# Kernel optimization log

Measured on AMD Instinct MI355X. Metric: run time of the kernel, lower is better.

The kernel has to match this reference:

```python
import jax, jax.numpy as jnp
from jax import lax
import numpy as np

NC = 3              # immutable color channels
HIDDEN = 16         # hidden state channels
STATE = NC + HIDDEN # 19
PV = 5              # perception vectors per channel
PERC = PV * STATE   # 95
MID = 128


def setup_inputs() -> dict:
    key = jax.random.key(0)
    ks = jax.random.split(key, 7)
    x = jax.random.uniform(ks[0], (4, NC, 128, 128), dtype=jnp.float32)
    # grouped 3x3 conv: groups=STATE, 1 in-ch -> PV out-ch per group; OIHW kernel (95,1,3,3)
    Wp = jax.random.normal(ks[1], (PERC, 1, 3, 3), dtype=jnp.float32) * 0.1
    bp = jax.random.normal(ks[2], (PERC,), dtype=jnp.float32) * 0.01
    W1 = jax.random.normal(ks[3], (MID, PERC), dtype=jnp.float32) * 0.05
    b1 = jax.random.normal(ks[4], (MID,), dtype=jnp.float32) * 0.01
    W2 = jax.random.normal(ks[5], (HIDDEN, MID), dtype=jnp.float32) * 0.05
    b2 = jax.random.normal(ks[6], (HIDDEN,), dtype=jnp.float32) * 0.01
    return {"x": x, "Wp": Wp, "bp": bp, "W1": W1, "b1": b1, "W2": W2, "b2": b2, "steps": 16}


def _maxpool3x3(x):
    # 3x3 stride-1 pad-1 max pool over NCHW spatial dims
    return lax.reduce_window(x, -jnp.inf, lax.max,
                             (1, 1, 3, 3), (1, 1, 1, 1),
                             ((0, 0), (0, 0), (1, 1), (1, 1)))


def reference(x, Wp, bp, W1, b1, W2, b2, steps):
    N, _, H, W = x.shape
    state0 = jnp.concatenate([x, jnp.zeros((N, HIDDEN, H, W), x.dtype)], axis=1)

    def step(state, _):
        # depthwise/grouped 3x3 perception conv (groups = STATE)
        p = lax.conv_general_dilated(state, Wp, (1, 1), ((1, 1), (1, 1)),
                                     feature_group_count=STATE,
                                     dimension_numbers=("NCHW", "OIHW", "NCHW"))
        p = p + bp[None, :, None, None]
        # 1x1 conv -> LeakyReLU(0.2) -> 1x1 conv
        h = jnp.einsum("nchw,oc->nohw", p, W1) + b1[None, :, None, None]
        h = jnp.where(h >= 0, h, 0.2 * h)
        upd = jnp.einsum("nchw,oc->nohw", h, W2) + b2[None, :, None, None]
        # stochastic_update with p=1: mask = rand < 1 is always True -> plain add
        s = state.at[:, NC:].add(upd)
        # alive mask: maxpool of channel 4 > 0 gates all mutable channels
        alive = (_maxpool3x3(s[:, 4:5]) > 0).astype(s.dtype)
        s = s.at[:, NC:].multiply(alive)
        # sigmoid slice-assign on channel 4
        s = s.at[:, 4].set(jax.nn.sigmoid(s[:, 4]))
        return s, None

    final, _ = lax.scan(step, state0, None, length=steps)
    return final
```

## Files before the change

### kernel.cpp

```cpp
#include <hip/hip_runtime.h>
#include <math.h>

#define NN    4
#define NC    3
#define HID   16
#define CST   19
#define PV    5
#define PERC  95
#define MIDC  128
#define HH    128
#define WW    128
#define HW    (HH*WW)
#define STEPS 16
#define TPX   256
#define NTHR  1024
#define KP    104
#define HT    136
#define W1F_N 24576
#define W2F_N 4096

typedef short  bf16x8 __attribute__((ext_vector_type(8)));
typedef float  f32x4v __attribute__((ext_vector_type(4)));

__device__ __forceinline__ unsigned short f2bf_rtn(float f) {
    unsigned u = __float_as_uint(f);
    u += 0x7FFFu + ((u >> 16) & 1u);
    return (unsigned short)(u >> 16);
}
__device__ __forceinline__ float bf2f(unsigned short h) {
    return __uint_as_float(((unsigned)h) << 16);
}
__device__ __forceinline__ void bfsplit(float a, short& hi, short& lo) {
    unsigned short hb = f2bf_rtn(a);
    hi = (short)hb;
    lo = (short)f2bf_rtn(a - bf2f(hb));
}
__device__ __forceinline__ unsigned packsplit(float a) {
    unsigned short hb = f2bf_rtn(a);
    unsigned short lb = f2bf_rtn(a - bf2f(hb));
    return ((unsigned)hb << 16) | (unsigned)lb;
}

__global__ __launch_bounds__(1024) void nca_wprep(
        short* __restrict__ wf,
        const float* __restrict__ W1, const float* __restrict__ W2) {
    const int tid = threadIdx.x;
    for (int e = tid; e < W1F_N; e += 1024) {
        int j = e & 7, lane = (e >> 3) & 63, q = e >> 9;
        int ch = q % 12, wrow = q / 12;
        int hl = ch & 1, t = ch >> 1, ks = t % 3, mt = t / 3;
        int lw = lane & 15, g = lane >> 4;
        int m  = wrow * 32 + mt * 16 + lw;
        int kk = ks * 32 + g * 8 + j;
        float av = (kk < PERC) ? W1[m * PERC + kk] : 0.0f;
        short hi, lo; bfsplit(av, hi, lo);
        wf[e] = hl ? lo : hi;
    }
    for (int e = tid; e < W2F_N; e += 1024) {
        int j = e & 7, lane = (e >> 3) & 63, q = e >> 9;
        int hl = q & 1, ks = q >> 1;
        int lw = lane & 15, g = lane >> 4;
        float av = W2[lw * MIDC + ks * 32 + g * 8 + j];
        short hi, lo; bfsplit(av, hi, lo);
        wf[W1F_N + e] = hl ? lo : hi;
    }
}

__global__ __launch_bounds__(NTHR) void nca_fused(
        const float* __restrict__ tmp_in,  long istride,
        float* __restrict__ tmp_out,       long ostride,
        const float* __restrict__ x,
        const short* __restrict__ wscr,
        const float* __restrict__ Wp, const float* __restrict__ bp,
        const float* __restrict__ b1, const float* __restrict__ b2,
        int first) {
    const int tile    = ((blockIdx.x & 7) << 5) + (blockIdx.x >> 3);
    const int n       = tile >> 6;
    const int pixbase = (tile & 63) * TPX;
    const int y0      = pixbase >> 7;
    const int tid     = threadIdx.x;
    const int lane    = tid & 63;
    const int w       = __builtin_amdgcn_readfirstlane(tid >> 6);
    const int wrow    = w >> 2;
    const int wcol    = w & 3;
    const int lw      = lane & 15;
    const int g       = lane >> 4;
    const int g8      = g * 8;

    __shared__ __align__(16) unsigned char raw[139840];
    unsigned* pp    = (unsigned*)raw;
    unsigned* hp    = (unsigned*)raw;
    float*    stile = (float*)(raw + 106496);
    float*    b1tab = (float*)(raw + 139264);
    float*    b2tab = (float*)(raw + 139776);

    if (tid < MIDC) b1tab[tid] = b1[tid];
    else if (tid < MIDC + HID) b2tab[tid - MIDC] = b2[tid - MIDC];

    {
        const int u2   = tid & 511;
        const int half = tid >> 9;
        const int px   = u2 & 127;
        const int yy   = y0 - 1 + (u2 >> 7);
        if (!first && yy >= 0 && yy < HH) {
            const float* tb = tmp_in + (size_t)n * istride;
            const float* c1 = tb + 1 * HW;
            const int idx = (yy << 7) + px;
            const bool ym = (yy > 0), yp = (yy < HH - 1);
            const bool xm = (px > 0), xp = (px < WW - 1);
            float mx = c1[idx];
            if (ym)       mx = fmaxf(mx, c1[idx - WW]);
            if (yp)       mx = fmaxf(mx, c1[idx + WW]);
            if (xm)       mx = fmaxf(mx, c1[idx - 1]);
            if (xp)       mx = fmaxf(mx, c1[idx + 1]);
            if (ym && xm) mx = fmaxf(mx, c1[idx - WW - 1]);
            if (ym && xp) mx = fmaxf(mx, c1[idx - WW + 1]);
            if (yp && xm) mx = fmaxf(mx, c1[idx + WW - 1]);
            if (yp && xp) mx = fmaxf(mx, c1[idx + WW + 1]);
            const float alive = (mx > 0.0f) ? 1.0f : 0.0f;
#pragma unroll
            for (int cc = 0; cc < 8; ++cc) {
                const int c = half * 8 + cc;
                float v = tb[c * HW + idx] * alive;
                if (c == 1) v = 1.0f / (1.0f + expf(-v));
                stile[c * 512 + u2] = v;
            }
        } else {
#pragma unroll
            for (int cc = 0; cc < 8; ++cc)
                stile[(half * 8 + cc) * 512 + u2] = 0.0f;
        }
    }

    bf16x8 ah[2][3], al[2][3];
#pragma unroll
    for (int mt = 0; mt < 2; ++mt)
#pragma unroll
        for (int ks = 0; ks < 3; ++ks) {
            const int base = ((wrow * 12 + ((mt * 3 + ks) << 1)) * 64 + lane) * 8;
            ah[mt][ks] = *(const bf16x8*)&wscr[base];
            al[mt][ks] = *(const bf16x8*)&wscr[base + 512];
        }

    auto conv_emit = [&](int c, int p, float t00, float t01, float t02,
                         float t10, float t11, float t12,
                         float t20, float t21, float t22) {
#pragma unroll
        for (int v = 0; v < PV; ++v) {
            const float* wv = Wp + (c * PV + v) * 9;
            float a = bp[c * PV + v];
            a += wv[0] * t00; a += wv[1] * t01; a += wv[2] * t02;
            a += wv[3] * t10; a += wv[4] * t11; a += wv[5] * t12;
            a += wv[6] * t20; a += wv[7] * t21; a += wv[8] * t22;
            pp[p * KP + c * PV + v] = packsplit(a);
        }
    };

    if (tid < 768) {
        const int c = tid >> 8;
        const int p = tid & 255;
        const int y = y0 + (p >> 7);
        const int xc = p & 127;
        const bool xm = (xc > 0), xp = (xc < WW - 1);
        const int gpix = (y << 7) + xc;
        const float* ch = x + ((size_t)n * NC + c) * HW;
        const bool ym = (y > 0), yp = (y < HH - 1);
        float t00 = (ym && xm) ? ch[gpix - WW - 1] : 0.0f;
        float t01 = ym         ? ch[gpix - WW]     : 0.0f;
        float t02 = (ym && xp) ? ch[gpix - WW + 1] : 0.0f;
        float t10 = xm         ? ch[gpix - 1]      : 0.0f;
        float t11 =              ch[gpix];
        float t12 = xp         ? ch[gpix + 1]      : 0.0f;
        float t20 = (yp && xm) ? ch[gpix + WW - 1] : 0.0f;
        float t21 = yp         ? ch[gpix + WW]     : 0.0f;
        float t22 = (yp && xp) ? ch[gpix + WW + 1] : 0.0f;
        conv_emit(c, p, t00, t01, t02, t10, t11, t12, t20, t21, t22);
    }
    if (tid < 256) pp[tid * KP + 95] = 0;
    __syncthreads();

#pragma unroll
    for (int it = 0; it < 4; ++it) {
        const int u = 768 + it * NTHR + tid;
        const int c = u >> 8;
        const int p = u & 255;
        const int xc = p & 127;
        const bool xm = (xc > 0), xp = (xc < WW - 1);
        const float* sr = stile + (c - NC) * 512;
        const int b = ((p >> 7) + 1) * 128 + xc;
        float t00 = xm ? sr[b - 128 - 1] : 0.0f;
        float t01 =      sr[b - 128];
        float t02 = xp ? sr[b - 128 + 1] : 0.0f;
        float t10 = xm ? sr[b - 1]       : 0.0f;
        float t11 =      sr[b];
        float t12 = xp ? sr[b + 1]       : 0.0f;
        float t20 = xm ? sr[b + 128 - 1] : 0.0f;
        float t21 =      sr[b + 128];
        float t22 = xp ? sr[b + 128 + 1] : 0.0f;
        conv_emit(c, p, t00, t01, t02, t10, t11, t12, t20, t21, t22);
    }
    __syncthreads();

    f32x4v acc[2][4];
#pragma unroll
    for (int mt = 0; mt < 2; ++mt)
#pragma unroll
        for (int nt = 0; nt < 4; ++nt)
            acc[mt][nt] = (f32x4v){0.0f, 0.0f, 0.0f, 0.0f};

    const int pxb = wcol * 64;
#pragma unroll
    for (int nt = 0; nt < 4; ++nt) {
#pragma unroll
        for (int ks = 0; ks < 3; ++ks) {
            const unsigned* pq = &pp[(pxb + nt * 16 + lw) * KP + ks * 32 + g8];
            uint4 qa = *(const uint4*)pq;
            uint4 qb = *(const uint4*)(pq + 4);
            const unsigned q[8] = {qa.x, qa.y, qa.z, qa.w,
                                   qb.x, qb.y, qb.z, qb.w};
            bf16x8 bh, bl;
#pragma unroll
            for (int j = 0; j < 8; ++j) {
                bh[j] = (short)(q[j] >> 16);
                bl[j] = (short)(q[j] & 0xffffu);
            }
            acc[0][nt] = __builtin_amdgcn_mfma_f32_16x16x32_bf16(ah[0][ks], bh, acc[0][nt], 0, 0, 0);
            acc[1][nt] = __builtin_amdgcn_mfma_f32_16x16x32_bf16(ah[1][ks], bh, acc[1][nt], 0, 0, 0);
            acc[0][nt] = __builtin_amdgcn_mfma_f32_16x16x32_bf16(ah[0][ks], bl, acc[0][nt], 0, 0, 0);
            acc[1][nt] = __builtin_amdgcn_mfma_f32_16x16x32_bf16(ah[1][ks], bl, acc[1][nt], 0, 0, 0);
            acc[0][nt] = __builtin_amdgcn_mfma_f32_16x16x32_bf16(al[0][ks], bh, acc[0][nt], 0, 0, 0);
            acc[1][nt] = __builtin_amdgcn_mfma_f32_16x16x32_bf16(al[1][ks], bh, acc[1][nt], 0, 0, 0);
        }
    }

#pragma unroll
    for (int mt = 0; mt < 2; ++mt) {
        f32x4v bq = *(const f32x4v*)&b1tab[wrow * 32 + mt * 16 + g * 4];
#pragma unroll
        for (int nt = 0; nt < 4; ++nt)
#pragma unroll
            for (int r = 0; r < 4; ++r) {
                float v = acc[mt][nt][r] + bq[r];
                acc[mt][nt][r] = (v >= 0.0f) ? v : 0.2f * v;
            }
    }

    float resid[4];
    {
        const int pxe = w * 16 + lw;
#pragma unroll
        for (int r = 0; r < 4; ++r)
            resid[r] = stile[(g * 4 + r) * 512 + (1 + (pxe >> 7)) * 128 + (pxe & 127)];
    }
    __syncthreads();

#pragma unroll
    for (int mt = 0; mt < 2; ++mt)
#pragma unroll
        for (int nt = 0; nt < 4; ++nt) {
            const int px = pxb + nt * 16 + lw;
            uint4 hv;
            hv.x = packsplit(acc[mt][nt][0]);
            hv.y = packsplit(acc[mt][nt][1]);
            hv.z = packsplit(acc[mt][nt][2]);
            hv.w = packsplit(acc[mt][nt][3]);
            *(uint4*)&hp[px * HT + wrow * 32 + mt * 16 + g * 4] = hv;
        }
    bf16x8 wh[4], wl[4];
    {
        const short* w2f = wscr + W1F_N;
#pragma unroll
        for (int ks = 0; ks < 4; ++ks) {
            const int base = ((ks * 2) * 64 + lane) * 8;
            wh[ks] = *(const bf16x8*)&w2f[base];
            wl[ks] = *(const bf16x8*)&w2f[base + 512];
        }
    }
    __syncthreads();

    f32x4v acc2 = (f32x4v){0.0f, 0.0f, 0.0f, 0.0f};
#pragma unroll
    for (int ks = 0; ks < 4; ++ks) {
        const unsigned* hq = &hp[(w * 16 + lw) * HT + ks * 32 + g8];
        uint4 qa = *(const uint4*)hq;
        uint4 qb = *(const uint4*)(hq + 4);
        const unsigned q[8] = {qa.x, qa.y, qa.z, qa.w,
                               qb.x, qb.y, qb.z, qb.w};
        bf16x8 bh, bl;
#pragma unroll
        for (int j = 0; j < 8; ++j) {
            bh[j] = (short)(q[j] >> 16);
            bl[j] = (short)(q[j] & 0xffffu);
        }
        acc2 = __builtin_amdgcn_mfma_f32_16x16x32_bf16(wh[ks], bh, acc2, 0, 0, 0);
        acc2 = __builtin_amdgcn_mfma_f32_16x16x32_bf16(wl[ks], bh, acc2, 0, 0, 0);
        acc2 = __builtin_amdgcn_mfma_f32_16x16x32_bf16(wh[ks], bl, acc2, 0, 0, 0);
    }

    {
        const int px = w * 16 + lw;
        const int gp = pixbase + px;
        float* tb = tmp_out + (size_t)n * ostride;
#pragma unroll
        for (int r = 0; r < 4; ++r) {
            const int o = g * 4 + r;
            tb[(size_t)o * HW + gp] = acc2[r] + b2tab[o] + resid[r];
        }
    }
}

__global__ __launch_bounds__(256) void nca_step2(
        float* __restrict__ state,
        const float* __restrict__ tmp,
        const float* __restrict__ x) {
    int gid = blockIdx.x * 256 + threadIdx.x;
    int xx = gid & (WW - 1);
    int y = (gid >> 7) & (HH - 1);
    int n = gid >> 14;
    const int idx = y * WW + xx;

    const float* c4 = tmp + (size_t)n * HID * HW + 1 * HW;
    const bool ym = (y > 0), yp = (y < HH - 1);
    const bool xm = (xx > 0), xp = (xx < WW - 1);

    float mx = c4[idx];
    if (ym)       mx = fmaxf(mx, c4[idx - WW]);
    if (yp)       mx = fmaxf(mx, c4[idx + WW]);
    if (xm)       mx = fmaxf(mx, c4[idx - 1]);
    if (xp)       mx = fmaxf(mx, c4[idx + 1]);
    if (ym && xm) mx = fmaxf(mx, c4[idx - WW - 1]);
    if (ym && xp) mx = fmaxf(mx, c4[idx - WW + 1]);
    if (yp && xm) mx = fmaxf(mx, c4[idx + WW - 1]);
    if (yp && xp) mx = fmaxf(mx, c4[idx + WW + 1]);

    float alive = (mx > 0.0f) ? 1.0f : 0.0f;

    float* sb = state + (size_t)n * CST * HW + NC * HW + idx;
    const float* tb = tmp + (size_t)n * HID * HW + idx;
#pragma unroll
    for (int i = 0; i < HID; ++i) {
        float v = tb[i * HW] * alive;
        if (i == 1) v = 1.0f / (1.0f + expf(-v));
        sb[i * HW] = v;
    }
    float* cb = state + (size_t)n * CST * HW + idx;
#pragma unroll
    for (int c = 0; c < NC; ++c)
        cb[(size_t)c * HW] = x[((size_t)n * NC + c) * HW + idx];
}

extern "C" void kernel_launch(void* const* d_in, const int* in_sizes, int n_in,
                              void* d_out, int out_size, void* d_ws, size_t ws_size,
                              hipStream_t stream) {
    const float* x  = (const float*)d_in[0];
    const float* Wp = (const float*)d_in[1];
    const float* bp = (const float*)d_in[2];
    const float* W1 = (const float*)d_in[3];
    const float* b1 = (const float*)d_in[4];
    const float* W2 = (const float*)d_in[5];
    const float* b2 = (const float*)d_in[6];

    float* state = (float*)d_out;
    float* ws    = (float*)d_ws;

    short* wscr = (short*)state;

    float* bufA = state + (size_t)NC * HW;
    const long strideA = (long)CST * HW;
    float* bufB = ws;
    const long strideB = (long)HID * HW;

    nca_wprep<<<1, 1024, 0, stream>>>(wscr, W1, W2);

    const int blocks1 = (NN * HW) / TPX;
    for (int s = 0; s < STEPS; ++s) {
        const float* tin;  long sin;
        float*       tout; long sout;
        if ((s & 1) == 0) { tin = bufB; sin = strideB; tout = bufA; sout = strideA; }
        else              { tin = bufA; sin = strideA; tout = bufB; sout = strideB; }
        nca_fused<<<blocks1, NTHR, 0, stream>>>(tin, sin, tout, sout,
                                                x, wscr, Wp, bp, b1, b2,
                                                (s == 0) ? 1 : 0);
    }
    nca_step2<<<(NN * HW) / 256, 256, 0, stream>>>(state, ws, x);
}
```

Baseline: 312.6 us.

## Keep MLP hidden activations in registers and shuffle via ds_bpermute instead of LDS

Each wave now owns 16 pixels and computes all 128 hidden channels for them, instead of a 2D split of channels by pixels. The hidden activations stay in registers and are rearranged into the second GEMM's B-operand layout with ds_bpermute lane shuffles. This drops the LDS round trip for the hidden tensor and two __syncthreads barriers. In exchange, every wave reloads the full W1 fragments from global memory and issues many bpermute operations, and register pressure goes up.

```diff
diff --git a/kernel.cpp b/kernel.cpp
--- a/kernel.cpp
+++ b/kernel.cpp
@@ -15,7 +15,6 @@
 #define TPX   256
 #define NTHR  1024
 #define KP    104
-#define HT    136
 #define W1F_N 24576
 #define W2F_N 4096
 
@@ -81,15 +80,12 @@
     const int tid     = threadIdx.x;
     const int lane    = tid & 63;
     const int w       = __builtin_amdgcn_readfirstlane(tid >> 6);
-    const int wrow    = w >> 2;
-    const int wcol    = w & 3;
     const int lw      = lane & 15;
     const int g       = lane >> 4;
     const int g8      = g * 8;
 
     __shared__ __align__(16) unsigned char raw[139840];
     unsigned* pp    = (unsigned*)raw;
-    unsigned* hp    = (unsigned*)raw;
     float*    stile = (float*)(raw + 106496);
     float*    b1tab = (float*)(raw + 139264);
     float*    b2tab = (float*)(raw + 139776);
@@ -132,16 +128,6 @@
         }
     }
 
-    bf16x8 ah[2][3], al[2][3];
-#pragma unroll
-    for (int mt = 0; mt < 2; ++mt)
-#pragma unroll
-        for (int ks = 0; ks < 3; ++ks) {
-            const int base = ((wrow * 12 + ((mt * 3 + ks) << 1)) * 64 + lane) * 8;
-            ah[mt][ks] = *(const bf16x8*)&wscr[base];
-            al[mt][ks] = *(const bf16x8*)&wscr[base + 512];
-        }
-
     auto conv_emit = [&](int c, int p, float t00, float t01, float t02,
                          float t10, float t11, float t12,
                          float t20, float t21, float t22) {
@@ -201,100 +187,70 @@
     }
     __syncthreads();
 
-    f32x4v acc[2][4];
-#pragma unroll
-    for (int mt = 0; mt < 2; ++mt)
-#pragma unroll
-        for (int nt = 0; nt < 4; ++nt)
-            acc[mt][nt] = (f32x4v){0.0f, 0.0f, 0.0f, 0.0f};
-
-    const int pxb = wcol * 64;
-#pragma unroll
-    for (int nt = 0; nt < 4; ++nt) {
-#pragma unroll
-        for (int ks = 0; ks < 3; ++ks) {
-            const unsigned* pq = &pp[(pxb + nt * 16 + lw) * KP + ks * 32 + g8];
-            uint4 qa = *(const uint4*)pq;
-            uint4 qb = *(const uint4*)(pq + 4);
-            const unsigned q[8] = {qa.x, qa.y, qa.z, qa.w,
-                                   qb.x, qb.y, qb.z, qb.w};
-            bf16x8 bh, bl;
-#pragma unroll
-            for (int j = 0; j < 8; ++j) {
-                bh[j] = (short)(q[j] >> 16);
-                bl[j] = (short)(q[j] & 0xffffu);
-            }
-            acc[0][nt] = __builtin_amdgcn_mfma_f32_16x16x32_bf16(ah[0][ks], bh, acc[0][nt], 0, 0, 0);
-            acc[1][nt] = __builtin_amdgcn_mfma_f32_16x16x32_bf16(ah[1][ks], bh, acc[1][nt], 0, 0, 0);
-            acc[0][nt] = __builtin_amdgcn_mfma_f32_16x16x32_bf16(ah[0][ks], bl, acc[0][nt], 0, 0, 0);
-            acc[1][nt] = __builtin_amdgcn_mfma_f32_16x16x32_bf16(ah[1][ks], bl, acc[1][nt], 0, 0, 0);
-            acc[0][nt] = __builtin_amdgcn_mfma_f32_16x16x32_bf16(al[0][ks], bh, acc[0][nt], 0, 0, 0);
-            acc[1][nt] = __builtin_amdgcn_mfma_f32_16x16x32_bf16(al[1][ks], bh, acc[1][nt], 0, 0, 0);
-        }
-    }
-
-#pragma unroll
-    for (int mt = 0; mt < 2; ++mt) {
-        f32x4v bq = *(const f32x4v*)&b1tab[wrow * 32 + mt * 16 + g * 4];
-#pragma unroll
-        for (int nt = 0; nt < 4; ++nt)
-#pragma unroll
-            for (int r = 0; r < 4; ++r) {
-                float v = acc[mt][nt][r] + bq[r];
-                acc[mt][nt][r] = (v >= 0.0f) ? v : 0.2f * v;
-            }
-    }
-
-    float resid[4];
-    {
-        const int pxe = w * 16 + lw;
-#pragma unroll
-        for (int r = 0; r < 4; ++r)
-            resid[r] = stile[(g * 4 + r) * 512 + (1 + (pxe >> 7)) * 128 + (pxe & 127)];
-    }
-    __syncthreads();
-
-#pragma unroll
-    for (int mt = 0; mt < 2; ++mt)
-#pragma unroll
-        for (int nt = 0; nt < 4; ++nt) {
-            const int px = pxb + nt * 16 + lw;
-            uint4 hv;
-            hv.x = packsplit(acc[mt][nt][0]);
-            hv.y = packsplit(acc[mt][nt][1]);
-            hv.z = packsplit(acc[mt][nt][2]);
-            hv.w = packsplit(acc[mt][nt][3]);
-            *(uint4*)&hp[px * HT + wrow * 32 + mt * 16 + g * 4] = hv;
-        }
-    bf16x8 wh[4], wl[4];
-    {
-        const short* w2f = wscr + W1F_N;
-#pragma unroll
-        for (int ks = 0; ks < 4; ++ks) {
-            const int base = ((ks * 2) * 64 + lane) * 8;
-            wh[ks] = *(const bf16x8*)&w2f[base];
-            wl[ks] = *(const bf16x8*)&w2f[base + 512];
-        }
-    }
-    __syncthreads();
-
-    f32x4v acc2 = (f32x4v){0.0f, 0.0f, 0.0f, 0.0f};
-#pragma unroll
-    for (int ks = 0; ks < 4; ++ks) {
-        const unsigned* hq = &hp[(w * 16 + lw) * HT + ks * 32 + g8];
-        uint4 qa = *(const uint4*)hq;
-        uint4 qb = *(const uint4*)(hq + 4);
+    bf16x8 bh[3], bl[3];
+#pragma unroll
+    for (int ks = 0; ks < 3; ++ks) {
+        const unsigned* pq = &pp[(w * 16 + lw) * KP + ks * 32 + g8];
+        uint4 qa = *(const uint4*)pq;
+        uint4 qb = *(const uint4*)(pq + 4);
         const unsigned q[8] = {qa.x, qa.y, qa.z, qa.w,
                                qb.x, qb.y, qb.z, qb.w};
-        bf16x8 bh, bl;
 #pragma unroll
         for (int j = 0; j < 8; ++j) {
-            bh[j] = (short)(q[j] >> 16);
-            bl[j] = (short)(q[j] & 0xffffu);
-        }
-        acc2 = __builtin_amdgcn_mfma_f32_16x16x32_bf16(wh[ks], bh, acc2, 0, 0, 0);
-        acc2 = __builtin_amdgcn_mfma_f32_16x16x32_bf16(wl[ks], bh, acc2, 0, 0, 0);
-        acc2 = __builtin_amdgcn_mfma_f32_16x16x32_bf16(wh[ks], bl, acc2, 0, 0, 0);
+            bh[ks][j] = (short)(q[j] >> 16);
+            bl[ks][j] = (short)(q[j] & 0xffffu);
+        }
+    }
+
+    unsigned pk[8][4];
+#pragma unroll
+    for (int mt = 0; mt < 8; ++mt) {
+        f32x4v acc = (f32x4v){0.0f, 0.0f, 0.0f, 0.0f};
+#pragma unroll
+        for (int ks = 0; ks < 3; ++ks) {
+            const int base = (((mt >> 1) * 12 + (((mt & 1) * 3 + ks) << 1)) * 64
+                              + lane) * 8;
+            bf16x8 ah = *(const bf16x8*)&wscr[base];
+            bf16x8 al = *(const bf16x8*)&wscr[base + 512];
+            acc = __builtin_amdgcn_mfma_f32_16x16x32_bf16(ah, bh[ks], acc, 0, 0, 0);
+            acc = __builtin_amdgcn_mfma_f32_16x16x32_bf16(ah, bl[ks], acc, 0, 0, 0);
+            acc = __builtin_amdgcn_mfma_f32_16x16x32_bf16(al, bh[ks], acc, 0, 0, 0);
+        }
+        f32x4v bq = *(const f32x4v*)&b1tab[mt * 16 + g * 4];
+#pragma unroll
+        for (int r = 0; r < 4; ++r) {
+            float v = acc[r] + bq[r];
+            v = (v >= 0.0f) ? v : 0.2f * v;
+            pk[mt][r] = packsplit(v);
+        }
+    }
+
+    const int addrA = (lw + ((g & 1) << 5)) << 2;
+    const int addrB = addrA + 64;
+    const bool ghi = (g >= 2);
+    f32x4v acc2 = (f32x4v){0.0f, 0.0f, 0.0f, 0.0f};
+    const short* w2f = wscr + W1F_N;
+#pragma unroll
+    for (int ks = 0; ks < 4; ++ks) {
+        bf16x8 wh = *(const bf16x8*)&w2f[((ks * 2) * 64 + lane) * 8];
+        bf16x8 wl = *(const bf16x8*)&w2f[((ks * 2 + 1) * 64 + lane) * 8];
+        bf16x8 b2h, b2l;
+#pragma unroll
+        for (int r = 0; r < 4; ++r) {
+            int vA0 = __builtin_amdgcn_ds_bpermute(addrA, (int)pk[2 * ks][r]);
+            int vA1 = __builtin_amdgcn_ds_bpermute(addrA, (int)pk[2 * ks + 1][r]);
+            unsigned v0 = (unsigned)(ghi ? vA1 : vA0);
+            int vB0 = __builtin_amdgcn_ds_bpermute(addrB, (int)pk[2 * ks][r]);
+            int vB1 = __builtin_amdgcn_ds_bpermute(addrB, (int)pk[2 * ks + 1][r]);
+            unsigned v1 = (unsigned)(ghi ? vB1 : vB0);
+            b2h[r]     = (short)(v0 >> 16);
+            b2l[r]     = (short)(v0 & 0xffffu);
+            b2h[4 + r] = (short)(v1 >> 16);
+            b2l[4 + r] = (short)(v1 & 0xffffu);
+        }
+        acc2 = __builtin_amdgcn_mfma_f32_16x16x32_bf16(wh, b2h, acc2, 0, 0, 0);
+        acc2 = __builtin_amdgcn_mfma_f32_16x16x32_bf16(wl, b2h, acc2, 0, 0, 0);
+        acc2 = __builtin_amdgcn_mfma_f32_16x16x32_bf16(wh, b2l, acc2, 0, 0, 0);
     }
 
     {
@@ -304,7 +260,8 @@
 #pragma unroll
         for (int r = 0; r < 4; ++r) {
             const int o = g * 4 + r;
-            tb[(size_t)o * HW + gp] = acc2[r] + b2tab[o] + resid[r];
+            float resid = stile[o * 512 + (1 + (px >> 7)) * 128 + (px & 127)];
+            tb[(size_t)o * HW + gp] = acc2[r] + b2tab[o] + resid;
         }
     }
 }
```

Result: no change. 318.2 us (+1.8%).
